# Performance work log

Hardware: AMD Instinct MI355X
Metric: run time of the kernel (lower is better)

## Reference

```python
import jax, jax.numpy as jnp
import numpy as np


def setup_inputs() -> dict:
    key = jax.random.key(0)
    ks = jax.random.split(key, 5)
    S, B, I, H = 512, 64, 512, 512
    scale_in = 1.0 / np.sqrt(I)
    scale_h = 1.0 / np.sqrt(H)
    return {
        "x": jax.random.normal(ks[0], (S, B, I), dtype=jnp.float32),
        "W1": jax.random.normal(ks[1], (H, I), dtype=jnp.float32) * scale_in,
        "b1": jax.random.normal(ks[2], (H,), dtype=jnp.float32) * scale_in,
        "W2": jax.random.normal(ks[3], (H, H), dtype=jnp.float32) * scale_h,
        "b2": jax.random.normal(ks[4], (H,), dtype=jnp.float32) * scale_h,
    }


def reference(x, W1, b1, W2, b2):
    # Elman RNN: h_t = tanh(x_t @ W1^T + b1 + h_{t-1} @ W2^T + b2)
    # Precompute the input projection for all timesteps in one big GEMM.
    # x: [S, B, I] -> xp: [S, B, H]
    xp = jnp.einsum('sbi,hi->sbh', x, W1) + b1
    B, H = x.shape[1], W2.shape[0]
    h0 = jnp.zeros((B, H), dtype=x.dtype)

    def step(h, xp_t):
        h_new = jnp.tanh(xp_t + h @ W2.T + b2)
        return h_new, h_new

    h_last, h_seq = jax.lax.scan(step, h0, xp)
    return h_seq, h_last
```

## Files before the change

### kernel.cpp

```cpp
#include <hip/hip_runtime.h>
#include <math.h>

#define SS 512
#define BB 64
#define II 512
#define HH 512
#define MM (SS*BB)
#define HXC_WORDS ((size_t)SS * BB * 256)
#define HXC_BYTES (HXC_WORDS * 4)

typedef _Float16 h2 __attribute__((ext_vector_type(2)));
typedef _Float16 f16x8 __attribute__((ext_vector_type(8)));
typedef float f32x4 __attribute__((ext_vector_type(4)));

__device__ __forceinline__ h2 bc_h2(unsigned u) { return __builtin_bit_cast(h2, u); }
__device__ __forceinline__ unsigned bc_u(h2 v) { return __builtin_bit_cast(unsigned, v); }
__device__ __forceinline__ h2 pk(float x, float y) {
    return __builtin_bit_cast(h2, __builtin_amdgcn_cvt_pkrtz(x, y));
}

#if __has_builtin(__builtin_amdgcn_exp2f)
#define EXP2F __builtin_amdgcn_exp2f
#else
#define EXP2F exp2f
#endif
#if __has_builtin(__builtin_amdgcn_rcpf)
#define RCPF __builtin_amdgcn_rcpf
#else
#define RCPF(x) (1.0f / (x))
#endif

__device__ __forceinline__ float fast_tanh(float z) {
    float e = EXP2F(z * 2.885390081777927f);
    return 1.0f - 2.0f * RCPF(e + 1.0f);
}

__device__ __forceinline__ void bar_lds() {
    asm volatile("s_waitcnt lgkmcnt(0)\n\ts_barrier" ::: "memory");
}

__global__ __launch_bounds__(256) void k_ingemm2(const float* __restrict__ X,
                                                 const float* __restrict__ W1,
                                                 const float* __restrict__ b1,
                                                 float* __restrict__ C) {
    __shared__ __align__(16) _Float16 As[128 * 32];
    __shared__ __align__(16) _Float16 Bs[128 * 32];
    const int bm = blockIdx.x * 128;
    const int bn = blockIdx.y * 128;
    const int t = threadIdx.x;
    const int lane = t & 63;
    const int w = t >> 6;
    const int srow = t >> 1;
    const int kb0 = (t & 1) * 32;
    const int wm = (w >> 1) * 64, wn = (w & 1) * 64;

    f32x4 acc[4][4];
#pragma unroll
    for (int i = 0; i < 4; i++)
#pragma unroll
        for (int j = 0; j < 4; j++) acc[i][j] = f32x4{0.f, 0.f, 0.f, 0.f};

    const float* xs = X + (size_t)(bm + srow) * II + (t & 1) * 16;
    const float* ws = W1 + (size_t)(bn + srow) * II + (t & 1) * 16;
    char* asb = (char*)As + srow * 64;
    char* bsb = (char*)Bs + srow * 64;
    const int sw = (srow & 3) << 4;

    const int frow = lane & 15;
    const int fkb = (lane >> 4) * 16;
    const int fsw = (frow & 3) << 4;

    for (int kt = 0; kt < 16; ++kt) {
        float4 a0 = *(const float4*)(xs + kt * 32 + 0);
        float4 a1 = *(const float4*)(xs + kt * 32 + 4);
        float4 a2 = *(const float4*)(xs + kt * 32 + 8);
        float4 a3 = *(const float4*)(xs + kt * 32 + 12);
        float4 c0 = *(const float4*)(ws + kt * 32 + 0);
        float4 c1 = *(const float4*)(ws + kt * 32 + 4);
        float4 c2 = *(const float4*)(ws + kt * 32 + 8);
        float4 c3 = *(const float4*)(ws + kt * 32 + 12);
        __syncthreads();
        uint4 u0, u1, v0, v1;
        u0.x = bc_u(pk(a0.x, a0.y)); u0.y = bc_u(pk(a0.z, a0.w));
        u0.z = bc_u(pk(a1.x, a1.y)); u0.w = bc_u(pk(a1.z, a1.w));
        u1.x = bc_u(pk(a2.x, a2.y)); u1.y = bc_u(pk(a2.z, a2.w));
        u1.z = bc_u(pk(a3.x, a3.y)); u1.w = bc_u(pk(a3.z, a3.w));
        v0.x = bc_u(pk(c0.x, c0.y)); v0.y = bc_u(pk(c0.z, c0.w));
        v0.z = bc_u(pk(c1.x, c1.y)); v0.w = bc_u(pk(c1.z, c1.w));
        v1.x = bc_u(pk(c2.x, c2.y)); v1.y = bc_u(pk(c2.z, c2.w));
        v1.z = bc_u(pk(c3.x, c3.y)); v1.w = bc_u(pk(c3.z, c3.w));
        *(uint4*)(asb + ((kb0 + 0) ^ sw)) = u0;
        *(uint4*)(asb + ((kb0 + 16) ^ sw)) = u1;
        *(uint4*)(bsb + ((kb0 + 0) ^ sw)) = v0;
        *(uint4*)(bsb + ((kb0 + 16) ^ sw)) = v1;
        __syncthreads();

        f16x8 af[4], bf[4];
#pragma unroll
        for (int i = 0; i < 4; i++) {
            const int ar = wm + 16 * i + frow;
            af[i] = *(const f16x8*)((const char*)As + ar * 64 + (fkb ^ fsw));
            const int br = wn + 16 * i + frow;
            bf[i] = *(const f16x8*)((const char*)Bs + br * 64 + (fkb ^ fsw));
        }
#pragma unroll
        for (int i = 0; i < 4; i++)
#pragma unroll
            for (int j = 0; j < 4; j++)
                acc[i][j] = __builtin_amdgcn_mfma_f32_16x16x32_f16(
                    af[i], bf[j], acc[i][j], 0, 0, 0);
    }

    const int erow = bm + wm + (lane >> 4) * 4;
    const int ecol = bn + wn + (lane & 15);
#pragma unroll
    for (int j = 0; j < 4; j++) {
        const float bj = b1[ecol + 16 * j];
#pragma unroll
        for (int i = 0; i < 4; i++)
#pragma unroll
            for (int r = 0; r < 4; r++)
                C[(size_t)(erow + 16 * i + r) * HH + ecol + 16 * j] =
                    acc[i][j][r] + bj;
    }
}

__global__ __attribute__((amdgpu_flat_work_group_size(512, 512)))
__attribute__((amdgpu_waves_per_eu(2, 2)))
void k_rec9(const float* __restrict__ W2,
            const float* __restrict__ b2,
            float* __restrict__ out,
            float* __restrict__ hlast,
            unsigned* __restrict__ hxc) {
    const int wgid = blockIdx.x;
    const int b = wgid & 63;
    const int half = wgid >> 6;
    const int t = threadIdx.x;
    const int lane = t & 63;
    const int wv = t >> 6;
    const int colbase = half << 8;

    __shared__ float part[8][256];
    __shared__ __align__(4) _Float16 hsmem[256];
    const unsigned* hs32 = (const unsigned*)hsmem;

    h2 wreg[4][32];
    {
        const int pown = (half << 7) + (wv << 4);
        const int popp = ((1 - half) << 7) + (wv << 4);
#pragma unroll
        for (int ci = 0; ci < 4; ci++) {
            const float2* wrow =
                (const float2*)(W2 + (size_t)(colbase + lane + (ci << 6)) * HH);
#pragma unroll
            for (int g = 0; g < 16; g++) {
                float2 f = wrow[pown + g];
                wreg[ci][g] = pk(f.x, f.y);
            }
#pragma unroll
            for (int g = 0; g < 16; g++) {
                float2 f = wrow[popp + g];
                wreg[ci][16 + g] = pk(f.x, f.y);
            }
        }
    }
    if (t < 256) hsmem[t] = (_Float16)0.0f;
    float bias = 0.f;
    if (t < 256) bias = b2[colbase + t];
    float* po = out + (size_t)b * HH + colbase + t;
    const unsigned* rd = hxc + (size_t)b * 256 + ((1 - half) << 7) +
                         (wv << 4) + (lane & 15);
    unsigned* wr = hxc + (size_t)b * 256 + (half << 7) + (t >> 1);
    float hn = 0.0f;
    __syncthreads();

    for (int s = 0; s < SS; ++s) {
        float xpv = 0.f;
        if (t < 256) xpv = *po;

        unsigned hv1 = hs32[(wv << 4) + (lane & 15)];
        h2 aA[4], aB[4];
#pragma unroll
        for (int ci = 0; ci < 4; ci++) { aA[ci] = h2{0, 0}; aB[ci] = h2{0, 0}; }
#pragma unroll
        for (int g = 0; g < 16; g++) {
            h2 hp = bc_h2((unsigned)__builtin_amdgcn_readlane((int)hv1, g));
            if (g & 1) {
                aB[0] += wreg[0][g] * hp; aB[1] += wreg[1][g] * hp;
                aB[2] += wreg[2][g] * hp; aB[3] += wreg[3][g] * hp;
            } else {
                aA[0] += wreg[0][g] * hp; aA[1] += wreg[1][g] * hp;
                aA[2] += wreg[2][g] * hp; aA[3] += wreg[3][g] * hp;
            }
        }

        unsigned hv2 = 0;
        if (s > 0) {
            const unsigned* p = rd + (size_t)(s - 1) * (BB * 256);
            do {
                hv2 = __hip_atomic_load(p, __ATOMIC_RELAXED,
                                        __HIP_MEMORY_SCOPE_AGENT);
            } while (hv2 == 0xFFFFFFFFu);
        }
#pragma unroll
        for (int g = 0; g < 16; g++) {
            h2 hp = bc_h2((unsigned)__builtin_amdgcn_readlane((int)hv2, g));
            if (g & 1) {
                aB[0] += wreg[0][16 + g] * hp; aB[1] += wreg[1][16 + g] * hp;
                aB[2] += wreg[2][16 + g] * hp; aB[3] += wreg[3][16 + g] * hp;
            } else {
                aA[0] += wreg[0][16 + g] * hp; aA[1] += wreg[1][16 + g] * hp;
                aA[2] += wreg[2][16 + g] * hp; aA[3] += wreg[3][16 + g] * hp;
            }
        }
#pragma unroll
        for (int ci = 0; ci < 4; ci++) {
            h2 sv = aA[ci] + aB[ci];
            part[wv][lane + (ci << 6)] = (float)sv.x + (float)sv.y;
        }
        bar_lds();

        if (t < 256) {
            float z = part[0][t] + part[1][t] + part[2][t] + part[3][t] +
                      part[4][t] + part[5][t] + part[6][t] + part[7][t] +
                      bias + xpv;
            hn = fast_tanh(z);
            *po = hn;
            hsmem[t] = (_Float16)hn;
            float ho = __shfl_xor(hn, 1);
            if (!(t & 1)) {
                __hip_atomic_store(wr + (size_t)s * (BB * 256),
                                   bc_u(pk(hn, ho)),
                                   __ATOMIC_RELAXED, __HIP_MEMORY_SCOPE_AGENT);
            }
        }
        po += BB * HH;
        bar_lds();
    }
    if (t < 256) hlast[(size_t)b * HH + colbase + t] = hn;
}

__global__ __attribute__((amdgpu_flat_work_group_size(512, 512)))
__attribute__((amdgpu_waves_per_eu(2, 2)))
void k_rec8(const float* __restrict__ W2,
            const float* __restrict__ b2,
            float* __restrict__ out,
            float* __restrict__ hlast) {
    const int b = blockIdx.x;
    const int t = threadIdx.x;
    const int lane = t & 63;
    const int w = t >> 6;

    __shared__ uint4 wlds[16][512];
    __shared__ float part[8][512];
    __shared__ __align__(4) _Float16 hsmem[HH];
    const unsigned* hs32 = (const unsigned*)hsmem;

    h2 wreg[6][32];
#pragma unroll
    for (int ci = 0; ci < 6; ci++) {
        const float2* src =
            (const float2*)(W2 + (size_t)(lane + 64 * ci) * HH) + (w << 5);
#pragma unroll
        for (int g = 0; g < 32; g++) wreg[ci][g] = pk(src[g].x, src[g].y);
    }
#pragma unroll
    for (int cc = 0; cc < 2; cc++) {
        const float2* src =
            (const float2*)(W2 + (size_t)(lane + 384 + 64 * cc) * HH) + (w << 5);
#pragma unroll
        for (int q = 0; q < 8; q++) {
            uint4 u;
            u.x = bc_u(pk(src[4 * q + 0].x, src[4 * q + 0].y));
            u.y = bc_u(pk(src[4 * q + 1].x, src[4 * q + 1].y));
            u.z = bc_u(pk(src[4 * q + 2].x, src[4 * q + 2].y));
            u.w = bc_u(pk(src[4 * q + 3].x, src[4 * q + 3].y));
            wlds[cc * 8 + q][t] = u;
        }
    }
    hsmem[t] = (_Float16)0.0f;
    const float bias = b2[t];
    float* po = out + (size_t)b * HH + t;
    float hn = 0.0f;
    __syncthreads();

    for (int step = 0; step < SS; ++step) {
        float xpv = *po;
        unsigned hv = hs32[(w << 5) + (lane & 31)];

        h2 accA[8], accB[8];
#pragma unroll
        for (int c = 0; c < 8; c++) { accA[c] = h2{0, 0}; accB[c] = h2{0, 0}; }
#pragma unroll
        for (int q = 0; q < 8; q++) {
            uint4 u6 = wlds[q][t];
            uint4 u7 = wlds[8 + q][t];
            unsigned w6[4] = {u6.x, u6.y, u6.z, u6.w};
            unsigned w7[4] = {u7.x, u7.y, u7.z, u7.w};
#pragma unroll
            for (int gg = 0; gg < 4; gg++) {
                const int g = 4 * q + gg;
                h2 hp = bc_h2((unsigned)__builtin_amdgcn_readlane((int)hv, g));
                if (gg & 1) {
                    accB[0] += wreg[0][g] * hp; accB[1] += wreg[1][g] * hp;
                    accB[2] += wreg[2][g] * hp; accB[3] += wreg[3][g] * hp;
                    accB[4] += wreg[4][g] * hp; accB[5] += wreg[5][g] * hp;
                    accB[6] += bc_h2(w6[gg]) * hp;
                    accB[7] += bc_h2(w7[gg]) * hp;
                } else {
                    accA[0] += wreg[0][g] * hp; accA[1] += wreg[1][g] * hp;
                    accA[2] += wreg[2][g] * hp; accA[3] += wreg[3][g] * hp;
                    accA[4] += wreg[4][g] * hp; accA[5] += wreg[5][g] * hp;
                    accA[6] += bc_h2(w6[gg]) * hp;
                    accA[7] += bc_h2(w7[gg]) * hp;
                }
            }
        }
#pragma unroll
        for (int c = 0; c < 8; c++) {
            h2 s = accA[c] + accB[c];
            part[w][lane + 64 * c] = (float)s.x + (float)s.y;
        }
        bar_lds();

        float z = part[0][t] + part[1][t] + part[2][t] + part[3][t] +
                  part[4][t] + part[5][t] + part[6][t] + part[7][t] +
                  bias + xpv;
        hn = fast_tanh(z);
        hsmem[t] = (_Float16)hn;
        *po = hn;
        po += BB * HH;
        bar_lds();
    }
    hlast[(size_t)b * HH + t] = hn;
}

extern "C" void kernel_launch(void* const* d_in, const int* in_sizes, int n_in,
                              void* d_out, int out_size, void* d_ws, size_t ws_size,
                              hipStream_t stream) {
    const float* x  = (const float*)d_in[0];
    const float* W1 = (const float*)d_in[1];
    const float* b1 = (const float*)d_in[2];
    const float* W2 = (const float*)d_in[3];
    const float* b2 = (const float*)d_in[4];
    float* out = (float*)d_out;

    k_ingemm2<<<dim3(MM / 128, HH / 128), 256, 0, stream>>>(x, W1, b1, out);
    if (ws_size >= HXC_BYTES) {
        unsigned* hxc = (unsigned*)d_ws;
        hipMemsetAsync(d_ws, 0xFF, HXC_BYTES, stream);
        k_rec9<<<128, 512, 0, stream>>>(W2, b2, out,
                                        out + (size_t)SS * BB * HH, hxc);
    } else {
        k_rec8<<<BB, 512, 0, stream>>>(W2, b2, out, out + (size_t)SS * BB * HH);
    }
}
```

Measured before the change: 711.3 us.

## Exchange partial sums instead of hidden states between paired recurrence workgroups

Each workgroup now multiplies only its own half of the hidden state by both its own and its partner's weight columns. It publishes the packed fp16 partial sums for the partner's outputs, then computes its own-column partials while the exchange is in flight, and waits on the partner's contribution only just before the tanh. This moves the cross-workgroup wait off the critical path at the start of each step and overlaps it with local compute. The cost is an extra LDS reduction and barrier per step, plus fp16 rounding of the exchanged partial sums, which may reduce accuracy.

```diff
diff --git a/kernel.cpp b/kernel.cpp
--- a/kernel.cpp
+++ b/kernel.cpp
@@ -127,11 +127,11 @@
 
 __global__ __attribute__((amdgpu_flat_work_group_size(512, 512)))
 __attribute__((amdgpu_waves_per_eu(2, 2)))
-void k_rec9(const float* __restrict__ W2,
-            const float* __restrict__ b2,
-            float* __restrict__ out,
-            float* __restrict__ hlast,
-            unsigned* __restrict__ hxc) {
+void k_rec11(const float* __restrict__ W2,
+             const float* __restrict__ b2,
+             float* __restrict__ out,
+             float* __restrict__ hlast,
+             unsigned* __restrict__ hxc) {
     const int wgid = blockIdx.x;
     const int b = wgid & 63;
     const int half = wgid >> 6;
@@ -140,37 +140,33 @@
     const int wv = t >> 6;
     const int colbase = half << 8;
 
-    __shared__ float part[8][256];
+    __shared__ float partA[8][256];
+    __shared__ float partB[8][256];
     __shared__ __align__(4) _Float16 hsmem[256];
     const unsigned* hs32 = (const unsigned*)hsmem;
 
-    h2 wreg[4][32];
-    {
-        const int pown = (half << 7) + (wv << 4);
-        const int popp = ((1 - half) << 7) + (wv << 4);
-#pragma unroll
-        for (int ci = 0; ci < 4; ci++) {
-            const float2* wrow =
-                (const float2*)(W2 + (size_t)(colbase + lane + (ci << 6)) * HH);
-#pragma unroll
-            for (int g = 0; g < 16; g++) {
-                float2 f = wrow[pown + g];
-                wreg[ci][g] = pk(f.x, f.y);
-            }
-#pragma unroll
-            for (int g = 0; g < 16; g++) {
-                float2 f = wrow[popp + g];
-                wreg[ci][16 + g] = pk(f.x, f.y);
-            }
+    h2 wA[4][16], wB[4][16];
+#pragma unroll
+    for (int ci = 0; ci < 4; ci++) {
+        const int cA = ((1 - half) << 8) + lane + (ci << 6);
+        const int cB = colbase + lane + (ci << 6);
+        const float2* rA = (const float2*)(W2 + (size_t)cA * HH) +
+                           (half << 7) + (wv << 4);
+        const float2* rB = (const float2*)(W2 + (size_t)cB * HH) +
+                           (half << 7) + (wv << 4);
+#pragma unroll
+        for (int g = 0; g < 16; g++) {
+            wA[ci][g] = pk(rA[g].x, rA[g].y);
+            wB[ci][g] = pk(rB[g].x, rB[g].y);
         }
     }
     if (t < 256) hsmem[t] = (_Float16)0.0f;
     float bias = 0.f;
     if (t < 256) bias = b2[colbase + t];
     float* po = out + (size_t)b * HH + colbase + t;
-    const unsigned* rd = hxc + (size_t)b * 256 + ((1 - half) << 7) +
-                         (wv << 4) + (lane & 15);
-    unsigned* wr = hxc + (size_t)b * 256 + (half << 7) + (t >> 1);
+    unsigned* pub = hxc + (size_t)b * 256 + (half << 7) + t;
+    const unsigned* prb = hxc + (size_t)b * 256 + ((1 - half) << 7) +
+                          (t >> 1);
     float hn = 0.0f;
     __syncthreads();
 
@@ -178,61 +174,65 @@
         float xpv = 0.f;
         if (t < 256) xpv = *po;
 
-        unsigned hv1 = hs32[(wv << 4) + (lane & 15)];
-        h2 aA[4], aB[4];
-#pragma unroll
-        for (int ci = 0; ci < 4; ci++) { aA[ci] = h2{0, 0}; aB[ci] = h2{0, 0}; }
-#pragma unroll
-        for (int g = 0; g < 16; g++) {
-            h2 hp = bc_h2((unsigned)__builtin_amdgcn_readlane((int)hv1, g));
-            if (g & 1) {
-                aB[0] += wreg[0][g] * hp; aB[1] += wreg[1][g] * hp;
-                aB[2] += wreg[2][g] * hp; aB[3] += wreg[3][g] * hp;
-            } else {
-                aA[0] += wreg[0][g] * hp; aA[1] += wreg[1][g] * hp;
-                aA[2] += wreg[2][g] * hp; aA[3] += wreg[3][g] * hp;
+        unsigned hv = hs32[(wv << 4) + (lane & 15)];
+        {
+            h2 a0{0,0}, a1{0,0}, a2{0,0}, a3{0,0};
+#pragma unroll
+            for (int g = 0; g < 16; g++) {
+                h2 hp = bc_h2((unsigned)__builtin_amdgcn_readlane((int)hv, g));
+                a0 += wA[0][g] * hp; a1 += wA[1][g] * hp;
+                a2 += wA[2][g] * hp; a3 += wA[3][g] * hp;
             }
-        }
-
-        unsigned hv2 = 0;
-        if (s > 0) {
-            const unsigned* p = rd + (size_t)(s - 1) * (BB * 256);
-            do {
-                hv2 = __hip_atomic_load(p, __ATOMIC_RELAXED,
-                                        __HIP_MEMORY_SCOPE_AGENT);
-            } while (hv2 == 0xFFFFFFFFu);
-        }
-#pragma unroll
-        for (int g = 0; g < 16; g++) {
-            h2 hp = bc_h2((unsigned)__builtin_amdgcn_readlane((int)hv2, g));
-            if (g & 1) {
-                aB[0] += wreg[0][16 + g] * hp; aB[1] += wreg[1][16 + g] * hp;
-                aB[2] += wreg[2][16 + g] * hp; aB[3] += wreg[3][16 + g] * hp;
-            } else {
-                aA[0] += wreg[0][16 + g] * hp; aA[1] += wreg[1][16 + g] * hp;
-                aA[2] += wreg[2][16 + g] * hp; aA[3] += wreg[3][16 + g] * hp;
+            partA[wv][lane +   0] = (float)a0.x + (float)a0.y;
+            partA[wv][lane +  64] = (float)a1.x + (float)a1.y;
+            partA[wv][lane + 128] = (float)a2.x + (float)a2.y;
+            partA[wv][lane + 192] = (float)a3.x + (float)a3.y;
+        }
+        bar_lds();
+
+        if (t < 128) {
+            float s0 = 0.f, s1 = 0.f;
+#pragma unroll
+            for (int ks = 0; ks < 8; ks++) {
+                s0 += partA[ks][2 * t];
+                s1 += partA[ks][2 * t + 1];
             }
-        }
-#pragma unroll
-        for (int ci = 0; ci < 4; ci++) {
-            h2 sv = aA[ci] + aB[ci];
-            part[wv][lane + (ci << 6)] = (float)sv.x + (float)sv.y;
+            __hip_atomic_store(pub + (size_t)s * (BB * 256), bc_u(pk(s0, s1)),
+                               __ATOMIC_RELAXED, __HIP_MEMORY_SCOPE_AGENT);
+        }
+        unsigned pw = 0xFFFFFFFFu;
+        if (t < 256)
+            pw = __hip_atomic_load(prb + (size_t)s * (BB * 256),
+                                   __ATOMIC_RELAXED, __HIP_MEMORY_SCOPE_AGENT);
+
+        {
+            h2 a0{0,0}, a1{0,0}, a2{0,0}, a3{0,0};
+#pragma unroll
+            for (int g = 0; g < 16; g++) {
+                h2 hp = bc_h2((unsigned)__builtin_amdgcn_readlane((int)hv, g));
+                a0 += wB[0][g] * hp; a1 += wB[1][g] * hp;
+                a2 += wB[2][g] * hp; a3 += wB[3][g] * hp;
+            }
+            partB[wv][lane +   0] = (float)a0.x + (float)a0.y;
+            partB[wv][lane +  64] = (float)a1.x + (float)a1.y;
+            partB[wv][lane + 128] = (float)a2.x + (float)a2.y;
+            partB[wv][lane + 192] = (float)a3.x + (float)a3.y;
         }
         bar_lds();
 
         if (t < 256) {
-            float z = part[0][t] + part[1][t] + part[2][t] + part[3][t] +
-                      part[4][t] + part[5][t] + part[6][t] + part[7][t] +
-                      bias + xpv;
+            while (pw == 0xFFFFFFFFu)
+                pw = __hip_atomic_load(prb + (size_t)s * (BB * 256),
+                                       __ATOMIC_RELAXED,
+                                       __HIP_MEMORY_SCOPE_AGENT);
+            h2 pp = bc_h2(pw);
+            float pv = (t & 1) ? (float)pp.y : (float)pp.x;
+            float z = partB[0][t] + partB[1][t] + partB[2][t] + partB[3][t] +
+                      partB[4][t] + partB[5][t] + partB[6][t] + partB[7][t] +
+                      pv + bias + xpv;
             hn = fast_tanh(z);
             *po = hn;
             hsmem[t] = (_Float16)hn;
-            float ho = __shfl_xor(hn, 1);
-            if (!(t & 1)) {
-                __hip_atomic_store(wr + (size_t)s * (BB * 256),
-                                   bc_u(pk(hn, ho)),
-                                   __ATOMIC_RELAXED, __HIP_MEMORY_SCOPE_AGENT);
-            }
         }
         po += BB * HH;
         bar_lds();
@@ -349,8 +349,8 @@
     if (ws_size >= HXC_BYTES) {
         unsigned* hxc = (unsigned*)d_ws;
         hipMemsetAsync(d_ws, 0xFF, HXC_BYTES, stream);
-        k_rec9<<<128, 512, 0, stream>>>(W2, b2, out,
-                                        out + (size_t)SS * BB * HH, hxc);
+        k_rec11<<<128, 512, 0, stream>>>(W2, b2, out,
+                                         out + (size_t)SS * BB * HH, hxc);
     } else {
         k_rec8<<<BB, 512, 0, stream>>>(W2, b2, out, out + (size_t)SS * BB * HH);
     }
```

Result: slower. 804.7 us (+13.1%).
